# Kernel optimization log

Hardware: AMD Instinct MI355X
Metric: run time of the kernel (lower is better)

The kernel has to match this reference:

```python
import jax, jax.numpy as jnp
import numpy as np

B, C_IN, C_INTER, H, W_DIM = 8, 512, 256, 64, 64


def setup_inputs() -> dict:
    key = jax.random.key(0)
    k1, k2, k3, k4 = jax.random.split(key, 4)
    x = jax.random.normal(k1, (B, C_IN, H, W_DIM), dtype=jnp.float32)
    pem_feats = jax.random.normal(k2, (B, C_INTER, H * W_DIM), dtype=jnp.float32)
    # 1x1 conv weight stored as [out, in] (kernel spatial dims are 1x1)
    W = jax.random.normal(k3, (C_INTER, C_IN), dtype=jnp.float32) * (1.0 / np.sqrt(C_IN))
    bias = jax.random.normal(k4, (C_INTER,), dtype=jnp.float32) * 0.01
    return {"x": x, "pem_feats": pem_feats, "W": W, "bias": bias}


def reference(x, pem_feats, W, bias):
    b, c, h, w = x.shape
    # 1x1 conv == channel-mixing GEMM: [b, inter, h, w]
    proj = jnp.einsum('bchw,oc->bohw', x, W) + bias[None, :, None, None]
    proj = proj.reshape(b, -1, h * w)                      # [b, inter, hw]
    # weights[b,i,j] = <proj[:, i], pem[:, j]>  -> [b, hw, hw], softmax over j
    scores = jnp.einsum('bci,bcj->bij', proj, pem_feats)
    weights = jax.nn.softmax(scores, axis=-1)
    # out[b,k,i] = sum_j weights[b,j,i] * pem[b,k,j]
    eam = jnp.einsum('bji,bkj->bki', weights, pem_feats)   # [b, inter, hw]
    return eam.reshape(b, -1, h, w)
```

## Files before the change

### kernel.cpp

```cpp
#include <hip/hip_runtime.h>
#include <math.h>

#define BATCH 8
#define CIN 512
#define CO 256
#define HW 4096
#define KT 32
#define NSEG 4
#define SEGC 32

typedef unsigned short ushort_t;
typedef unsigned int uint_t;
typedef __bf16 v8bf __attribute__((ext_vector_type(8)));
typedef _Float16 v8h __attribute__((ext_vector_type(8)));
typedef _Float16 v4h __attribute__((ext_vector_type(4)));
typedef float v4f __attribute__((ext_vector_type(4)));
typedef ushort_t u16x8 __attribute__((ext_vector_type(8)));

__device__ __forceinline__ ushort_t f2bf(float f) {
  uint_t u = __float_as_uint(f);
  u += 0x7FFFu + ((u >> 16) & 1u);
  return (ushort_t)(u >> 16);
}
__device__ __forceinline__ float bf2f(ushort_t h) {
  return __uint_as_float(((uint_t)h) << 16);
}
__device__ __forceinline__ ushort_t f2h(float f) {
  return __builtin_bit_cast(ushort_t, (_Float16)f);
}
__device__ __forceinline__ v4f mfma16(v8bf a, v8bf b, v4f c) {
  return __builtin_amdgcn_mfma_f32_16x16x32_bf16(a, b, c, 0, 0, 0);
}
__device__ __forceinline__ v4f mfma16h(v8h a, v8h b, v4f c) {
  return __builtin_amdgcn_mfma_f32_16x16x32_f16(a, b, c, 0, 0, 0);
}
__device__ __forceinline__ v8h lds_frag_h512(const unsigned char* base, int row, int cb) {
  uint4 v = *(const uint4*)(base + row * 512 + (((cb) ^ (row & 7)) << 4));
  return __builtin_bit_cast(v8h, v);
}
__device__ __forceinline__ v8h lds_frag_h128(const unsigned char* base, int row, int cb) {
  uint4 v = *(const uint4*)(base + row * 128 + (((cb) ^ (row & 7)) << 4));
  return __builtin_bit_cast(v8h, v);
}
__device__ __forceinline__ v8bf lds_frag128(const unsigned char* base, int row, int cb) {
  uint4 v = *(const uint4*)(base + row * 128 + (((cb) ^ (row & 7)) << 4));
  return __builtin_bit_cast(v8bf, v);
}
__device__ __forceinline__ void gll16(const void* g, void* l) {
  __builtin_amdgcn_global_load_lds(
      (const __attribute__((address_space(1))) unsigned int*)g,
      (__attribute__((address_space(3))) unsigned int*)l, 16, 0, 0);
}

__global__ __launch_bounds__(256) void k_w_split(
    const float* __restrict__ W, ushort_t* __restrict__ w_hi,
    ushort_t* __restrict__ w_lo) {
  int idx = blockIdx.x * 256 + threadIdx.x;
  size_t off = (size_t)idx * 8;
  float4 v0 = *(const float4*)&W[off];
  float4 v1 = *(const float4*)&W[off + 4];
  float f[8] = {v0.x, v0.y, v0.z, v0.w, v1.x, v1.y, v1.z, v1.w};
  u16x8 h, l;
#pragma unroll
  for (int j = 0; j < 8; ++j) {
    ushort_t hh = f2bf(f[j]);
    h[j] = hh;
    l[j] = f2bf(f[j] - bf2f(hh));
  }
  *(u16x8*)&w_hi[off] = h;
  *(u16x8*)&w_lo[off] = l;
}

__global__ __launch_bounds__(256) void k_tr_x(
    const float* __restrict__ x,
    ushort_t* __restrict__ xt_hi, ushort_t* __restrict__ xt_lo) {
  __shared__ float T[64][65];
  const int i0 = blockIdx.x * 64;
  const int c0 = blockIdx.y * 64;
  const int b  = blockIdx.z;
  const int t  = threadIdx.x;
  const int cl = t >> 4;
  const int i4 = (t & 15) * 4;
#pragma unroll
  for (int r = 0; r < 4; ++r) {
    int c = c0 + r * 16 + cl;
    size_t off = ((size_t)b * CIN + c) * HW + i0 + i4;
    float4 v = *(const float4*)&x[off];
    T[r * 16 + cl][i4 + 0] = v.x;
    T[r * 16 + cl][i4 + 1] = v.y;
    T[r * 16 + cl][i4 + 2] = v.z;
    T[r * 16 + cl][i4 + 3] = v.w;
  }
  __syncthreads();
  {
    int il = t >> 2;
    int cs = (t & 3) * 16;
    u16x8 h0, h1, l0, l1;
#pragma unroll
    for (int j = 0; j < 8; ++j) {
      float f = T[cs + j][il];
      ushort_t h = f2bf(f);
      h0[j] = h;
      l0[j] = f2bf(f - bf2f(h));
    }
#pragma unroll
    for (int j = 0; j < 8; ++j) {
      float f = T[cs + 8 + j][il];
      ushort_t h = f2bf(f);
      h1[j] = h;
      l1[j] = f2bf(f - bf2f(h));
    }
    size_t ro = ((size_t)b * HW + i0 + il) * CIN + c0 + cs;
    *(u16x8*)&xt_hi[ro]     = h0;
    *(u16x8*)&xt_hi[ro + 8] = h1;
    *(u16x8*)&xt_lo[ro]     = l0;
    *(u16x8*)&xt_lo[ro + 8] = l1;
  }
}

__global__ __launch_bounds__(256, 2) void k_proj_mfma(
    const ushort_t* __restrict__ xt_hi, const ushort_t* __restrict__ xt_lo,
    const ushort_t* __restrict__ w_hi, const ushort_t* __restrict__ w_lo,
    const float* __restrict__ bias, ushort_t* __restrict__ proj_h) {
  __shared__ __align__(16) unsigned char L[4][128 * 128];
  const int bid = blockIdx.x;
  const int b = bid & 7;
  const int rest = bid >> 3;
  const int xt = rest & 31;
  const int oh = rest >> 5;
  const int x0 = xt * 128;
  const int t = threadIdx.x;
  const int lane = t & 63, wave = t >> 6;

  v4f acc[2][8];
#pragma unroll
  for (int xf = 0; xf < 2; ++xf)
#pragma unroll
    for (int of = 0; of < 8; ++of) acc[xf][of] = (v4f){0.f, 0.f, 0.f, 0.f};

  float bias_of[8];
#pragma unroll
  for (int of = 0; of < 8; ++of)
    bias_of[of] = bias[oh * 128 + of * 16 + (lane & 15)];

  for (int ch = 0; ch < 8; ++ch) {
    const int c0 = ch * 64;
#pragma unroll
    for (int i = 0; i < 4; ++i) {
      int G = i * 256 + t;
      int r = G >> 3, sl = G & 7;
      int cg = (sl ^ (r & 7)) << 3;
      size_t xsrc = ((size_t)b * HW + x0 + r) * CIN + c0 + cg;
      size_t wsrc = ((size_t)(oh * 128 + r)) * CIN + c0 + cg;
      unsigned lb = (unsigned)((i * 256 + wave * 64) << 4);
      gll16(&xt_hi[xsrc], &L[0][lb]);
      gll16(&xt_lo[xsrc], &L[1][lb]);
      gll16(&w_hi[wsrc],  &L[2][lb]);
      gll16(&w_lo[wsrc],  &L[3][lb]);
    }
    __syncthreads();
#pragma unroll
    for (int st = 0; st < 2; ++st) {
      int cb = st * 4 + (lane >> 4);
      v8bf ah0 = lds_frag128(L[0], wave * 32 + (lane & 15), cb);
      v8bf ah1 = lds_frag128(L[0], wave * 32 + 16 + (lane & 15), cb);
      v8bf al0 = lds_frag128(L[1], wave * 32 + (lane & 15), cb);
      v8bf al1 = lds_frag128(L[1], wave * 32 + 16 + (lane & 15), cb);
#pragma unroll
      for (int of = 0; of < 8; ++of) {
        v8bf bh = lds_frag128(L[2], of * 16 + (lane & 15), cb);
        v8bf bl = lds_frag128(L[3], of * 16 + (lane & 15), cb);
        acc[0][of] = mfma16(ah0, bh, acc[0][of]);
        acc[0][of] = mfma16(ah0, bl, acc[0][of]);
        acc[0][of] = mfma16(al0, bh, acc[0][of]);
        acc[1][of] = mfma16(ah1, bh, acc[1][of]);
        acc[1][of] = mfma16(ah1, bl, acc[1][of]);
        acc[1][of] = mfma16(al1, bh, acc[1][of]);
      }
    }
    __syncthreads();
  }

  ushort_t* Th = (ushort_t*)&L[0][0];
#pragma unroll
  for (int xf = 0; xf < 2; ++xf)
#pragma unroll
    for (int of = 0; of < 8; ++of)
#pragma unroll
      for (int r = 0; r < 4; ++r) {
        int x_loc = wave * 32 + xf * 16 + (lane >> 4) * 4 + r;
        int o_loc = of * 16 + (lane & 15);
        Th[x_loc * 128 + o_loc] = f2h(acc[xf][of][r] + bias_of[of]);
      }
  __syncthreads();
  {
    int row = t >> 1, half = t & 1;
    size_t off = ((size_t)b * HW + x0 + row) * CO + oh * 128 + half * 64;
#pragma unroll
    for (int j = 0; j < 8; ++j)
      *(uint4*)&proj_h[off + j * 8] =
          *(const uint4*)&Th[row * 128 + half * 64 + j * 8];
  }
}

__global__ __launch_bounds__(256) void k_tr_pem(
    const float* __restrict__ pem,
    ushort_t* __restrict__ pem_t_h, ushort_t* __restrict__ pem_h) {
  __shared__ float T[64][65];
  const int y0 = blockIdx.x * 64;
  const int c0 = blockIdx.y * 64;
  const int b  = blockIdx.z;
  const int t  = threadIdx.x;
  const int cl = t >> 4;
  const int y4 = (t & 15) * 4;
#pragma unroll
  for (int r = 0; r < 4; ++r) {
    int c = c0 + r * 16 + cl;
    size_t off = ((size_t)b * CO + c) * HW + y0 + y4;
    float4 v = *(const float4*)&pem[off];
    ushort4 h;
    h.x = f2h(v.x); h.y = f2h(v.y); h.z = f2h(v.z); h.w = f2h(v.w);
    *(ushort4*)&pem_h[off] = h;
    T[r * 16 + cl][y4 + 0] = v.x;
    T[r * 16 + cl][y4 + 1] = v.y;
    T[r * 16 + cl][y4 + 2] = v.z;
    T[r * 16 + cl][y4 + 3] = v.w;
  }
  __syncthreads();
  {
    int yl = t >> 2;
    int cs = (t & 3) * 16;
    u16x8 h0, h1;
#pragma unroll
    for (int j = 0; j < 8; ++j) h0[j] = f2h(T[cs + j][yl]);
#pragma unroll
    for (int j = 0; j < 8; ++j) h1[j] = f2h(T[cs + 8 + j][yl]);
    size_t ro = ((size_t)b * HW + y0 + yl) * CO + c0 + cs;
    *(u16x8*)&pem_t_h[ro]     = h0;
    *(u16x8*)&pem_t_h[ro + 8] = h1;
  }
}

__global__ __launch_bounds__(256, 2) void k_stats_f16(
    const ushort_t* __restrict__ proj_h, const ushort_t* __restrict__ pem_t_h,
    float* __restrict__ m_seg, float* __restrict__ d_seg) {
  __shared__ __align__(16) unsigned char pbuf[2][32 * 512];
  const int id = blockIdx.x;
  const int b = id & 7;
  const int rest = id >> 3;
  const int xt = rest & 15;
  const int seg = rest >> 4;
  const int x0 = xt * 256;
  const int t = threadIdx.x;
  const int lane = t & 63, wave = t >> 6;
  const int xw = x0 + wave * 64;

  v8h Ah[4][8];
#pragma unroll
  for (int xf = 0; xf < 4; ++xf) {
    const size_t ro =
        ((size_t)b * HW + xw + xf * 16 + (lane & 15)) * CO + (lane >> 4) * 8;
#pragma unroll
    for (int st = 0; st < 8; ++st)
      Ah[xf][st] = __builtin_bit_cast(v8h, *(const uint4*)&proj_h[ro + st * 32]);
  }

  float m[4][4], d[4][4];
#pragma unroll
  for (int xf = 0; xf < 4; ++xf)
#pragma unroll
    for (int r = 0; r < 4; ++r) { m[xf][r] = -3.0e38f; d[xf][r] = 0.f; }

  auto stage = [&](int bufi, int tt) {
    const int yy0 = tt * 32;
#pragma unroll
    for (int i = 0; i < 4; ++i) {
      int G = i * 256 + t;
      int r = G >> 5, sl = G & 31;
      size_t so = ((size_t)b * HW + yy0 + r) * CO + ((sl ^ (r & 7)) << 3);
      unsigned lb = (unsigned)((i * 256 + wave * 64) << 4);
      gll16(&pem_t_h[so], &pbuf[bufi][lb]);
    }
  };

  const int tt0 = seg * SEGC;
  stage(0, tt0);
  __syncthreads();

  for (int tc = 0; tc < SEGC; ++tc) {
    if (tc + 1 < SEGC) stage((tc + 1) & 1, tt0 + tc + 1);

    const unsigned char* bp = pbuf[tc & 1];
    v4f acc[4][2];
#pragma unroll
    for (int xf = 0; xf < 4; ++xf)
#pragma unroll
      for (int yc = 0; yc < 2; ++yc) acc[xf][yc] = (v4f){0.f, 0.f, 0.f, 0.f};

#pragma unroll
    for (int st = 0; st < 8; ++st) {
#pragma unroll
      for (int yc = 0; yc < 2; ++yc) {
        v8h bh = lds_frag_h512(bp, yc * 16 + (lane & 15), st * 4 + (lane >> 4));
        acc[0][yc] = mfma16h(Ah[0][st], bh, acc[0][yc]);
        acc[1][yc] = mfma16h(Ah[1][st], bh, acc[1][yc]);
        acc[2][yc] = mfma16h(Ah[2][st], bh, acc[2][yc]);
        acc[3][yc] = mfma16h(Ah[3][st], bh, acc[3][yc]);
      }
    }

#pragma unroll
    for (int xf = 0; xf < 4; ++xf) {
      float mx8 = fmaxf(fmaxf(fmaxf(acc[xf][0][0], acc[xf][0][1]),
                              fmaxf(acc[xf][0][2], acc[xf][0][3])),
                        fmaxf(fmaxf(acc[xf][1][0], acc[xf][1][1]),
                              fmaxf(acc[xf][1][2], acc[xf][1][3])));
      float minm = fminf(fminf(m[xf][0], m[xf][1]), fminf(m[xf][2], m[xf][3]));
      if (__any(mx8 > minm + 8.0f)) {
#pragma unroll
        for (int r = 0; r < 4; ++r) {
          float rm = fmaxf(acc[xf][0][r], acc[xf][1][r]);
          rm = fmaxf(rm, __shfl_xor(rm, 1));
          rm = fmaxf(rm, __shfl_xor(rm, 2));
          rm = fmaxf(rm, __shfl_xor(rm, 4));
          rm = fmaxf(rm, __shfl_xor(rm, 8));
          float mn = fmaxf(m[xf][r], rm);
          d[xf][r] *= __expf(m[xf][r] - mn);
          m[xf][r] = mn;
        }
      }
#pragma unroll
      for (int r = 0; r < 4; ++r)
        d[xf][r] += __expf(acc[xf][0][r] - m[xf][r]) +
                    __expf(acc[xf][1][r] - m[xf][r]);
    }
    __syncthreads();
  }

#pragma unroll
  for (int xf = 0; xf < 4; ++xf) {
    float dv[4];
#pragma unroll
    for (int r = 0; r < 4; ++r) {
      float v = d[xf][r];
      v += __shfl_xor(v, 1);
      v += __shfl_xor(v, 2);
      v += __shfl_xor(v, 4);
      v += __shfl_xor(v, 8);
      dv[r] = v;
    }
    if ((lane & 15) == 0) {
      size_t o = ((size_t)(b * NSEG + seg)) * HW + xw + xf * 16 + (lane >> 4) * 4;
      *(float4*)&m_seg[o] = make_float4(m[xf][0], m[xf][1], m[xf][2], m[xf][3]);
      *(float4*)&d_seg[o] = make_float4(dv[0], dv[1], dv[2], dv[3]);
    }
  }
}

__global__ __launch_bounds__(256) void k_red2(
    const float* __restrict__ m_seg, const float* __restrict__ d_seg,
    float* __restrict__ Cx) {
  int idx = blockIdx.x * 256 + threadIdx.x;
  int b = idx >> 12;
  int xx = idx & 4095;
  float ms[NSEG], ds[NSEG];
  float mm = -3.0e38f;
#pragma unroll
  for (int s = 0; s < NSEG; ++s) {
    ms[s] = m_seg[((size_t)(b * NSEG + s)) * HW + xx];
    ds[s] = d_seg[((size_t)(b * NSEG + s)) * HW + xx];
    mm = fmaxf(mm, ms[s]);
  }
  float dd = 0.f;
#pragma unroll
  for (int s = 0; s < NSEG; ++s) dd += ds[s] * __expf(ms[s] - mm);
  Cx[(size_t)b * HW + xx] = mm + __logf(dd);
}

__global__ __launch_bounds__(256, 2) void k_fused(
    const ushort_t* __restrict__ proj_h, const ushort_t* __restrict__ pem_t_h,
    const ushort_t* __restrict__ pem_h, const float* __restrict__ Cx,
    float* __restrict__ out) {
  __shared__ __align__(16) unsigned char Lp[64 * 512];
  __shared__ __align__(16) unsigned char Lk[256 * 128];
  __shared__ __align__(16) unsigned char Le[64 * 128];
  __shared__ float Clds[64];
  const int id = blockIdx.x;
  const int b = id & 7;
  const int yt = id >> 3;
  const int y0 = yt * 64;
  const int t = threadIdx.x;
  const int lane = t & 63, wave = t >> 6;

  v8h Bres[8];
  {
    const size_t ro =
        ((size_t)b * HW + y0 + wave * 16 + (lane & 15)) * CO + (lane >> 4) * 8;
#pragma unroll
    for (int st = 0; st < 8; ++st)
      Bres[st] = __builtin_bit_cast(v8h, *(const uint4*)&pem_t_h[ro + st * 32]);
  }

  v4f pv[4][4];
#pragma unroll
  for (int kf = 0; kf < 4; ++kf)
#pragma unroll
    for (int yf = 0; yf < 4; ++yf) pv[kf][yf] = (v4f){0.f, 0.f, 0.f, 0.f};

  for (int xt = 0; xt < 64; ++xt) {
    const int x0 = xt * 64;
    __syncthreads();
#pragma unroll
    for (int i = 0; i < 8; ++i) {
      int G = i * 256 + t;
      int r = G >> 5, sl = G & 31;
      size_t so = ((size_t)b * HW + x0 + r) * CO + ((sl ^ (r & 7)) << 3);
      gll16(&proj_h[so], &Lp[(unsigned)((i * 256 + wave * 64) << 4)]);
    }
#pragma unroll
    for (int i = 0; i < 8; ++i) {
      int G = i * 256 + t;
      int r = G >> 3, sl = G & 7;
      size_t so = ((size_t)b * CO + r) * HW + x0 + ((sl ^ (r & 7)) << 3);
      gll16(&pem_h[so], &Lk[(unsigned)((i * 256 + wave * 64) << 4)]);
    }
    if (t < 64) Clds[t] = Cx[(size_t)b * HW + x0 + t];
    __syncthreads();

    v4f s[4];
#pragma unroll
    for (int xf = 0; xf < 4; ++xf) s[xf] = (v4f){0.f, 0.f, 0.f, 0.f};
#pragma unroll
    for (int st = 0; st < 8; ++st) {
      int cb = st * 4 + (lane >> 4);
      v8h bh = Bres[st];
      s[0] = mfma16h(lds_frag_h512(Lp, 0  + (lane & 15), cb), bh, s[0]);
      s[1] = mfma16h(lds_frag_h512(Lp, 16 + (lane & 15), cb), bh, s[1]);
      s[2] = mfma16h(lds_frag_h512(Lp, 32 + (lane & 15), cb), bh, s[2]);
      s[3] = mfma16h(lds_frag_h512(Lp, 48 + (lane & 15), cb), bh, s[3]);
    }
    {
      int yl = wave * 16 + (lane & 15);
      int half = (lane >> 4) & 1;
      int gbase = (lane >> 4) >> 1;
#pragma unroll
      for (int xf = 0; xf < 4; ++xf) {
        float4 c4 = *(const float4*)&Clds[xf * 16 + (lane >> 4) * 4];
        float cc[4] = {c4.x, c4.y, c4.z, c4.w};
        v4h p;
#pragma unroll
        for (int r = 0; r < 4; ++r) p[r] = (_Float16)__expf(s[xf][r] - cc[r]);
        int gx = xf * 2 + gbase;
        *(uint2*)(Le + yl * 128 + ((gx ^ (yl & 7)) << 4) + half * 8) =
            __builtin_bit_cast(uint2, p);
      }
    }
    __syncthreads();

    const int kb = wave * 64;
#pragma unroll
    for (int ks = 0; ks < 2; ++ks) {
      int cb = ks * 4 + (lane >> 4);
      v8h e0 = lds_frag_h128(Le, 0  + (lane & 15), cb);
      v8h e1 = lds_frag_h128(Le, 16 + (lane & 15), cb);
      v8h e2 = lds_frag_h128(Le, 32 + (lane & 15), cb);
      v8h e3 = lds_frag_h128(Le, 48 + (lane & 15), cb);
#pragma unroll
      for (int kf = 0; kf < 4; ++kf) {
        v8h af = lds_frag_h128(Lk, kb + kf * 16 + (lane & 15), cb);
        pv[kf][0] = mfma16h(af, e0, pv[kf][0]);
        pv[kf][1] = mfma16h(af, e1, pv[kf][1]);
        pv[kf][2] = mfma16h(af, e2, pv[kf][2]);
        pv[kf][3] = mfma16h(af, e3, pv[kf][3]);
      }
    }
  }

#pragma unroll
  for (int kf = 0; kf < 4; ++kf)
#pragma unroll
    for (int yf = 0; yf < 4; ++yf)
#pragma unroll
      for (int r = 0; r < 4; ++r) {
        int k = wave * 64 + kf * 16 + (lane >> 4) * 4 + r;
        int y = y0 + yf * 16 + (lane & 15);
        out[((size_t)b * CO + k) * HW + y] = pv[kf][yf][r];
      }
}

__global__ __launch_bounds__(256) void k_proj(
    const float* __restrict__ x, const float* __restrict__ W,
    const float* __restrict__ bias, float* __restrict__ proj) {
  __shared__ float As[KT][68];
  __shared__ float Bs[KT][68];
  const int i0 = blockIdx.x * 64;
  const int o0 = blockIdx.y * 64;
  const int b  = blockIdx.z;
  const int t  = threadIdx.x;
  const int tx = t & 15, ty = t >> 4;
  const float* xb = x + (size_t)b * CIN * HW;
  float acc[4][4] = {};
  for (int c0 = 0; c0 < CIN; c0 += KT) {
#pragma unroll
    for (int l = 0; l < 8; ++l) {
      int idx = t + l * 256;
      int o = idx >> 5;
      int c = idx & 31;
      As[c][o] = W[(size_t)(o0 + o) * CIN + c0 + c];
    }
#pragma unroll
    for (int l = 0; l < 2; ++l) {
      int idx4 = t + l * 256;
      int c = idx4 >> 4;
      int i4 = idx4 & 15;
      *(float4*)&Bs[c][i4 * 4] =
          *(const float4*)&xb[(size_t)(c0 + c) * HW + i0 + i4 * 4];
    }
    __syncthreads();
#pragma unroll
    for (int c = 0; c < KT; ++c) {
      float4 a  = *(const float4*)&As[c][tx * 4];
      float4 bv = *(const float4*)&Bs[c][ty * 4];
      float av[4] = {a.x, a.y, a.z, a.w};
      float bb[4] = {bv.x, bv.y, bv.z, bv.w};
#pragma unroll
      for (int u = 0; u < 4; ++u)
#pragma unroll
        for (int v = 0; v < 4; ++v) acc[u][v] += av[u] * bb[v];
    }
    __syncthreads();
  }
  float* pbout = proj + (size_t)b * CO * HW;
#pragma unroll
  for (int u = 0; u < 4; ++u) {
    int o = o0 + tx * 4 + u;
    float bsv = bias[o];
    float4 r;
    r.x = acc[u][0] + bsv; r.y = acc[u][1] + bsv;
    r.z = acc[u][2] + bsv; r.w = acc[u][3] + bsv;
    *(float4*)&pbout[(size_t)o * HW + i0 + ty * 4] = r;
  }
}

__global__ __launch_bounds__(256) void k_stats(
    const float* __restrict__ proj, const float* __restrict__ pem,
    float* __restrict__ Mx, float* __restrict__ Dinv) {
  __shared__ float As[KT][68];
  __shared__ float Bs[KT][68];
  __shared__ float MsS[64][17];
  __shared__ float DsS[64][17];
  const int x0 = blockIdx.x * 64;
  const int b  = blockIdx.y;
  const int t  = threadIdx.x;
  const int tx = t & 15, ty = t >> 4;
  const float* pj = proj + (size_t)b * CO * HW;
  const float* pe = pem + (size_t)b * CO * HW;
  float m[4], d[4];
#pragma unroll
  for (int u = 0; u < 4; ++u) { m[u] = -3.0e38f; d[u] = 0.f; }
  for (int y0 = 0; y0 < HW; y0 += 64) {
    float s[4][4] = {};
    for (int c0 = 0; c0 < CO; c0 += KT) {
#pragma unroll
      for (int l = 0; l < 2; ++l) {
        int idx4 = t + l * 256;
        int c = idx4 >> 4, w4 = idx4 & 15;
        *(float4*)&As[c][w4 * 4] =
            *(const float4*)&pj[(size_t)(c0 + c) * HW + x0 + w4 * 4];
        *(float4*)&Bs[c][w4 * 4] =
            *(const float4*)&pe[(size_t)(c0 + c) * HW + y0 + w4 * 4];
      }
      __syncthreads();
#pragma unroll
      for (int c = 0; c < KT; ++c) {
        float4 a  = *(const float4*)&As[c][tx * 4];
        float4 bv = *(const float4*)&Bs[c][ty * 4];
        float av[4] = {a.x, a.y, a.z, a.w};
        float bb[4] = {bv.x, bv.y, bv.z, bv.w};
#pragma unroll
        for (int u = 0; u < 4; ++u)
#pragma unroll
          for (int v = 0; v < 4; ++v) s[u][v] += av[u] * bb[v];
      }
      __syncthreads();
    }
#pragma unroll
    for (int u = 0; u < 4; ++u) {
      float mv = fmaxf(fmaxf(s[u][0], s[u][1]), fmaxf(s[u][2], s[u][3]));
      if (mv > m[u]) { d[u] *= __expf(m[u] - mv); m[u] = mv; }
      d[u] += __expf(s[u][0] - m[u]) + __expf(s[u][1] - m[u]) +
              __expf(s[u][2] - m[u]) + __expf(s[u][3] - m[u]);
    }
  }
#pragma unroll
  for (int u = 0; u < 4; ++u) { MsS[tx * 4 + u][ty] = m[u]; DsS[tx * 4 + u][ty] = d[u]; }
  __syncthreads();
  if (t < 64) {
    float mm = -3.0e38f;
#pragma unroll
    for (int i = 0; i < 16; ++i) mm = fmaxf(mm, MsS[t][i]);
    float dd = 0.f;
#pragma unroll
    for (int i = 0; i < 16; ++i) dd += DsS[t][i] * __expf(MsS[t][i] - mm);
    Mx[(size_t)b * HW + x0 + t]   = mm;
    Dinv[(size_t)b * HW + x0 + t] = 1.0f / dd;
  }
}

__global__ __launch_bounds__(256) void k_out(
    const float* __restrict__ proj, const float* __restrict__ pem,
    const float* __restrict__ Mx, const float* __restrict__ Dinv,
    float* __restrict__ out) {
  __shared__ float As[KT][68];
  __shared__ float Bs[KT][68];
  __shared__ float E[64][68];
  const int y0 = blockIdx.x * 64;
  const int b  = blockIdx.y;
  const int t  = threadIdx.x;
  const int tx = t & 15, ty = t >> 4;
  const int kg = t >> 3, yg = t & 7;
  const float* pj = proj + (size_t)b * CO * HW;
  const float* pe = pem + (size_t)b * CO * HW;
  const float* Mb = Mx + (size_t)b * HW;
  const float* Db = Dinv + (size_t)b * HW;
  float acc[8][8] = {};
  for (int x0 = 0; x0 < HW; x0 += 64) {
    float s[4][4] = {};
    for (int c0 = 0; c0 < CO; c0 += KT) {
#pragma unroll
      for (int l = 0; l < 2; ++l) {
        int idx4 = t + l * 256;
        int c = idx4 >> 4, w4 = idx4 & 15;
        *(float4*)&As[c][w4 * 4] =
            *(const float4*)&pj[(size_t)(c0 + c) * HW + x0 + w4 * 4];
        *(float4*)&Bs[c][w4 * 4] =
            *(const float4*)&pe[(size_t)(c0 + c) * HW + y0 + w4 * 4];
      }
      __syncthreads();
#pragma unroll
      for (int c = 0; c < KT; ++c) {
        float4 a  = *(const float4*)&As[c][tx * 4];
        float4 bv = *(const float4*)&Bs[c][ty * 4];
        float av[4] = {a.x, a.y, a.z, a.w};
        float bb[4] = {bv.x, bv.y, bv.z, bv.w};
#pragma unroll
        for (int u = 0; u < 4; ++u)
#pragma unroll
          for (int v = 0; v < 4; ++v) s[u][v] += av[u] * bb[v];
      }
      __syncthreads();
    }
#pragma unroll
    for (int u = 0; u < 4; ++u) {
      int xr = x0 + tx * 4 + u;
      float mm = Mb[xr];
      float di = Db[xr];
      E[tx * 4 + u][ty * 4 + 0] = __expf(s[u][0] - mm) * di;
      E[tx * 4 + u][ty * 4 + 1] = __expf(s[u][1] - mm) * di;
      E[tx * 4 + u][ty * 4 + 2] = __expf(s[u][2] - mm) * di;
      E[tx * 4 + u][ty * 4 + 3] = __expf(s[u][3] - mm) * di;
    }
    __syncthreads();
    for (int xi = 0; xi < 64; xi += 4) {
      float4 p[8];
#pragma unroll
      for (int u = 0; u < 8; ++u)
        p[u] = *(const float4*)&pe[(size_t)(kg * 8 + u) * HW + x0 + xi];
#pragma unroll
      for (int j = 0; j < 4; ++j) {
        float4 e0 = *(const float4*)&E[xi + j][yg * 8];
        float4 e1 = *(const float4*)&E[xi + j][yg * 8 + 4];
        float evv[8] = {e0.x, e0.y, e0.z, e0.w, e1.x, e1.y, e1.z, e1.w};
#pragma unroll
        for (int u = 0; u < 8; ++u) {
          float a = (j == 0) ? p[u].x : (j == 1) ? p[u].y : (j == 2) ? p[u].z : p[u].w;
#pragma unroll
          for (int v = 0; v < 8; ++v) acc[u][v] += a * evv[v];
        }
      }
    }
    __syncthreads();
  }
#pragma unroll
  for (int u = 0; u < 8; ++u) {
    int k = kg * 8 + u;
    float4 r0, r1;
    r0.x = acc[u][0]; r0.y = acc[u][1]; r0.z = acc[u][2]; r0.w = acc[u][3];
    r1.x = acc[u][4]; r1.y = acc[u][5]; r1.z = acc[u][6]; r1.w = acc[u][7];
    float* ob = out + ((size_t)b * CO + k) * HW + y0 + yg * 8;
    *(float4*)&ob[0] = r0;
    *(float4*)&ob[4] = r1;
  }
}

extern "C" void kernel_launch(void* const* d_in, const int* in_sizes, int n_in,
                              void* d_out, int out_size, void* d_ws, size_t ws_size,
                              hipStream_t stream) {
  const float* x    = (const float*)d_in[0];
  const float* pem  = (const float*)d_in[1];
  const float* W    = (const float*)d_in[2];
  const float* bias = (const float*)d_in[3];
  float* out = (float*)d_out;

  const size_t NS   = (size_t)BATCH * HW * CO;
  const size_t NS2  = (size_t)BATCH * HW * CIN;
  const size_t HWB  = (size_t)BATCH * HW;
  const size_t SEGN = (size_t)BATCH * NSEG * HW;
  const size_t WN   = (size_t)CO * CIN;

  unsigned char* basep = (unsigned char*)d_ws;
  ushort_t* proj_h   = (ushort_t*)basep;
  ushort_t* pem_t_h  = proj_h + NS;
  ushort_t* pem_h    = pem_t_h + NS;
  float*    Cxp      = (float*)(pem_h + NS);
  float*    m_seg    = Cxp + HWB;
  float*    d_seg    = m_seg + SEGN;
  ushort_t* xt_hi    = (ushort_t*)(d_seg + SEGN);
  ushort_t* xt_lo    = xt_hi + NS2;
  ushort_t* w_hi     = xt_lo + NS2;
  ushort_t* w_lo     = w_hi + WN;

  const size_t need = 3 * NS * 2 + HWB * 4 + 2 * SEGN * 4 + 2 * NS2 * 2 + 2 * WN * 2;

  if (ws_size < need) {
    float* proj = (float*)d_ws;
    float* Mx2  = proj + NS;
    float* Di2  = Mx2 + HWB;
    const size_t need_f = (NS + 2 * HWB) * sizeof(float);
    if (ws_size < need_f) return;
    k_proj <<<dim3(HW / 64, CO / 64, BATCH), 256, 0, stream>>>(x, W, bias, proj);
    k_stats<<<dim3(HW / 64, BATCH),          256, 0, stream>>>(proj, pem, Mx2, Di2);
    k_out  <<<dim3(HW / 64, BATCH),          256, 0, stream>>>(proj, pem, Mx2, Di2, out);
    return;
  }

  k_w_split<<<64, 256, 0, stream>>>(W, w_hi, w_lo);
  k_tr_x<<<dim3(HW / 64, CIN / 64, BATCH), 256, 0, stream>>>(x, xt_hi, xt_lo);
  k_proj_mfma<<<512, 256, 0, stream>>>(xt_hi, xt_lo, w_hi, w_lo, bias, proj_h);
  k_tr_pem<<<dim3(HW / 64, CO / 64, BATCH), 256, 0, stream>>>(pem, pem_t_h, pem_h);

  k_stats_f16<<<512, 256, 0, stream>>>(proj_h, pem_t_h, m_seg, d_seg);
  k_red2<<<128, 256, 0, stream>>>(m_seg, d_seg, Cxp);
  k_fused<<<512, 256, 0, stream>>>(proj_h, pem_t_h, pem_h, Cxp, out);
}
```

Measured before the change: 369.8 us.

## Use single fp16 projection GEMM, widen attention blocks to 512 threads with double buffering

The split bf16 hi/lo projection (three MFMAs per tile) becomes a single fp16 MFMA path, which removes the lo buffers and two thirds of the projection math and traffic. k_stats_f16 and k_fused now run 512-thread blocks covering larger tiles. k_fused double-buffers the proj/pem LDS stages so the next tile loads during the PV MFMAs, and it reads Cx straight from global instead of staging it in LDS. Projection accuracy drops to fp16, and the larger LDS footprint may reduce occupancy.

```diff
diff --git a/kernel.cpp b/kernel.cpp
--- a/kernel.cpp
+++ b/kernel.cpp
@@ -11,25 +11,13 @@
 
 typedef unsigned short ushort_t;
 typedef unsigned int uint_t;
-typedef __bf16 v8bf __attribute__((ext_vector_type(8)));
 typedef _Float16 v8h __attribute__((ext_vector_type(8)));
 typedef _Float16 v4h __attribute__((ext_vector_type(4)));
 typedef float v4f __attribute__((ext_vector_type(4)));
 typedef ushort_t u16x8 __attribute__((ext_vector_type(8)));
 
-__device__ __forceinline__ ushort_t f2bf(float f) {
-  uint_t u = __float_as_uint(f);
-  u += 0x7FFFu + ((u >> 16) & 1u);
-  return (ushort_t)(u >> 16);
-}
-__device__ __forceinline__ float bf2f(ushort_t h) {
-  return __uint_as_float(((uint_t)h) << 16);
-}
 __device__ __forceinline__ ushort_t f2h(float f) {
   return __builtin_bit_cast(ushort_t, (_Float16)f);
-}
-__device__ __forceinline__ v4f mfma16(v8bf a, v8bf b, v4f c) {
-  return __builtin_amdgcn_mfma_f32_16x16x32_bf16(a, b, c, 0, 0, 0);
 }
 __device__ __forceinline__ v4f mfma16h(v8h a, v8h b, v4f c) {
   return __builtin_amdgcn_mfma_f32_16x16x32_f16(a, b, c, 0, 0, 0);
@@ -41,10 +29,6 @@
 __device__ __forceinline__ v8h lds_frag_h128(const unsigned char* base, int row, int cb) {
   uint4 v = *(const uint4*)(base + row * 128 + (((cb) ^ (row & 7)) << 4));
   return __builtin_bit_cast(v8h, v);
-}
-__device__ __forceinline__ v8bf lds_frag128(const unsigned char* base, int row, int cb) {
-  uint4 v = *(const uint4*)(base + row * 128 + (((cb) ^ (row & 7)) << 4));
-  return __builtin_bit_cast(v8bf, v);
 }
 __device__ __forceinline__ void gll16(const void* g, void* l) {
   __builtin_amdgcn_global_load_lds(
@@ -52,28 +36,21 @@
       (__attribute__((address_space(3))) unsigned int*)l, 16, 0, 0);
 }
 
-__global__ __launch_bounds__(256) void k_w_split(
-    const float* __restrict__ W, ushort_t* __restrict__ w_hi,
-    ushort_t* __restrict__ w_lo) {
+__global__ __launch_bounds__(256) void k_w(
+    const float* __restrict__ W, ushort_t* __restrict__ w_h) {
   int idx = blockIdx.x * 256 + threadIdx.x;
   size_t off = (size_t)idx * 8;
   float4 v0 = *(const float4*)&W[off];
   float4 v1 = *(const float4*)&W[off + 4];
   float f[8] = {v0.x, v0.y, v0.z, v0.w, v1.x, v1.y, v1.z, v1.w};
-  u16x8 h, l;
-#pragma unroll
-  for (int j = 0; j < 8; ++j) {
-    ushort_t hh = f2bf(f[j]);
-    h[j] = hh;
-    l[j] = f2bf(f[j] - bf2f(hh));
-  }
-  *(u16x8*)&w_hi[off] = h;
-  *(u16x8*)&w_lo[off] = l;
+  u16x8 h;
+#pragma unroll
+  for (int j = 0; j < 8; ++j) h[j] = f2h(f[j]);
+  *(u16x8*)&w_h[off] = h;
 }
 
 __global__ __launch_bounds__(256) void k_tr_x(
-    const float* __restrict__ x,
-    ushort_t* __restrict__ xt_hi, ushort_t* __restrict__ xt_lo) {
+    const float* __restrict__ x, ushort_t* __restrict__ xt_h) {
   __shared__ float T[64][65];
   const int i0 = blockIdx.x * 64;
   const int c0 = blockIdx.y * 64;
@@ -95,34 +72,21 @@
   {
     int il = t >> 2;
     int cs = (t & 3) * 16;
-    u16x8 h0, h1, l0, l1;
-#pragma unroll
-    for (int j = 0; j < 8; ++j) {
-      float f = T[cs + j][il];
-      ushort_t h = f2bf(f);
-      h0[j] = h;
-      l0[j] = f2bf(f - bf2f(h));
-    }
-#pragma unroll
-    for (int j = 0; j < 8; ++j) {
-      float f = T[cs + 8 + j][il];
-      ushort_t h = f2bf(f);
-      h1[j] = h;
-      l1[j] = f2bf(f - bf2f(h));
-    }
+    u16x8 h0, h1;
+#pragma unroll
+    for (int j = 0; j < 8; ++j) h0[j] = f2h(T[cs + j][il]);
+#pragma unroll
+    for (int j = 0; j < 8; ++j) h1[j] = f2h(T[cs + 8 + j][il]);
     size_t ro = ((size_t)b * HW + i0 + il) * CIN + c0 + cs;
-    *(u16x8*)&xt_hi[ro]     = h0;
-    *(u16x8*)&xt_hi[ro + 8] = h1;
-    *(u16x8*)&xt_lo[ro]     = l0;
-    *(u16x8*)&xt_lo[ro + 8] = l1;
+    *(u16x8*)&xt_h[ro]     = h0;
+    *(u16x8*)&xt_h[ro + 8] = h1;
   }
 }
 
 __global__ __launch_bounds__(256, 2) void k_proj_mfma(
-    const ushort_t* __restrict__ xt_hi, const ushort_t* __restrict__ xt_lo,
-    const ushort_t* __restrict__ w_hi, const ushort_t* __restrict__ w_lo,
+    const ushort_t* __restrict__ xt_h, const ushort_t* __restrict__ w_h,
     const float* __restrict__ bias, ushort_t* __restrict__ proj_h) {
-  __shared__ __align__(16) unsigned char L[4][128 * 128];
+  __shared__ __align__(16) unsigned char L[2][128 * 128];
   const int bid = blockIdx.x;
   const int b = bid & 7;
   const int rest = bid >> 3;
@@ -153,29 +117,20 @@
       size_t xsrc = ((size_t)b * HW + x0 + r) * CIN + c0 + cg;
       size_t wsrc = ((size_t)(oh * 128 + r)) * CIN + c0 + cg;
       unsigned lb = (unsigned)((i * 256 + wave * 64) << 4);
-      gll16(&xt_hi[xsrc], &L[0][lb]);
-      gll16(&xt_lo[xsrc], &L[1][lb]);
-      gll16(&w_hi[wsrc],  &L[2][lb]);
-      gll16(&w_lo[wsrc],  &L[3][lb]);
+      gll16(&xt_h[xsrc], &L[0][lb]);
+      gll16(&w_h[wsrc],  &L[1][lb]);
     }
     __syncthreads();
 #pragma unroll
     for (int st = 0; st < 2; ++st) {
       int cb = st * 4 + (lane >> 4);
-      v8bf ah0 = lds_frag128(L[0], wave * 32 + (lane & 15), cb);
-      v8bf ah1 = lds_frag128(L[0], wave * 32 + 16 + (lane & 15), cb);
-      v8bf al0 = lds_frag128(L[1], wave * 32 + (lane & 15), cb);
-      v8bf al1 = lds_frag128(L[1], wave * 32 + 16 + (lane & 15), cb);
+      v8h ah0 = lds_frag_h128(L[0], wave * 32 + (lane & 15), cb);
+      v8h ah1 = lds_frag_h128(L[0], wave * 32 + 16 + (lane & 15), cb);
 #pragma unroll
       for (int of = 0; of < 8; ++of) {
-        v8bf bh = lds_frag128(L[2], of * 16 + (lane & 15), cb);
-        v8bf bl = lds_frag128(L[3], of * 16 + (lane & 15), cb);
-        acc[0][of] = mfma16(ah0, bh, acc[0][of]);
-        acc[0][of] = mfma16(ah0, bl, acc[0][of]);
-        acc[0][of] = mfma16(al0, bh, acc[0][of]);
-        acc[1][of] = mfma16(ah1, bh, acc[1][of]);
-        acc[1][of] = mfma16(ah1, bl, acc[1][of]);
-        acc[1][of] = mfma16(al1, bh, acc[1][of]);
+        v8h bh = lds_frag_h128(L[1], of * 16 + (lane & 15), cb);
+        acc[0][of] = mfma16h(ah0, bh, acc[0][of]);
+        acc[1][of] = mfma16h(ah1, bh, acc[1][of]);
       }
     }
     __syncthreads();
@@ -241,16 +196,16 @@
   }
 }
 
-__global__ __launch_bounds__(256, 2) void k_stats_f16(
+__global__ __launch_bounds__(512, 2) void k_stats_f16(
     const ushort_t* __restrict__ proj_h, const ushort_t* __restrict__ pem_t_h,
     float* __restrict__ m_seg, float* __restrict__ d_seg) {
   __shared__ __align__(16) unsigned char pbuf[2][32 * 512];
   const int id = blockIdx.x;
   const int b = id & 7;
   const int rest = id >> 3;
-  const int xt = rest & 15;
-  const int seg = rest >> 4;
-  const int x0 = xt * 256;
+  const int xt = rest & 7;
+  const int seg = rest >> 3;
+  const int x0 = xt * 512;
   const int t = threadIdx.x;
   const int lane = t & 63, wave = t >> 6;
   const int xw = x0 + wave * 64;
@@ -274,11 +229,11 @@
   auto stage = [&](int bufi, int tt) {
     const int yy0 = tt * 32;
 #pragma unroll
-    for (int i = 0; i < 4; ++i) {
-      int G = i * 256 + t;
+    for (int i = 0; i < 2; ++i) {
+      int G = i * 512 + t;
       int r = G >> 5, sl = G & 31;
       size_t so = ((size_t)b * HW + yy0 + r) * CO + ((sl ^ (r & 7)) << 3);
-      unsigned lb = (unsigned)((i * 256 + wave * 64) << 4);
+      unsigned lb = (unsigned)((i * 512 + wave * 64) << 4);
       gll16(&pem_t_h[so], &pbuf[bufi][lb]);
     }
   };
@@ -377,18 +332,17 @@
   Cx[(size_t)b * HW + xx] = mm + __logf(dd);
 }
 
-__global__ __launch_bounds__(256, 2) void k_fused(
+__global__ __launch_bounds__(512, 2) void k_fused(
     const ushort_t* __restrict__ proj_h, const ushort_t* __restrict__ pem_t_h,
     const ushort_t* __restrict__ pem_h, const float* __restrict__ Cx,
     float* __restrict__ out) {
-  __shared__ __align__(16) unsigned char Lp[64 * 512];
-  __shared__ __align__(16) unsigned char Lk[256 * 128];
-  __shared__ __align__(16) unsigned char Le[64 * 128];
-  __shared__ float Clds[64];
+  __shared__ __align__(16) unsigned char Lp[2][64 * 512];
+  __shared__ __align__(16) unsigned char Lk[2][256 * 128];
+  __shared__ __align__(16) unsigned char Le[128 * 128];
   const int id = blockIdx.x;
   const int b = id & 7;
   const int yt = id >> 3;
-  const int y0 = yt * 64;
+  const int y0 = yt * 128;
   const int t = threadIdx.x;
   const int lane = t & 63, wave = t >> 6;
 
@@ -401,30 +355,35 @@
       Bres[st] = __builtin_bit_cast(v8h, *(const uint4*)&pem_t_h[ro + st * 32]);
   }
 
-  v4f pv[4][4];
-#pragma unroll
-  for (int kf = 0; kf < 4; ++kf)
-#pragma unroll
-    for (int yf = 0; yf < 4; ++yf) pv[kf][yf] = (v4f){0.f, 0.f, 0.f, 0.f};
-
-  for (int xt = 0; xt < 64; ++xt) {
+  v4f pv[2][8];
+#pragma unroll
+  for (int kf = 0; kf < 2; ++kf)
+#pragma unroll
+    for (int yf = 0; yf < 8; ++yf) pv[kf][yf] = (v4f){0.f, 0.f, 0.f, 0.f};
+
+  auto stage = [&](int bufi, int xt) {
     const int x0 = xt * 64;
-    __syncthreads();
-#pragma unroll
-    for (int i = 0; i < 8; ++i) {
-      int G = i * 256 + t;
+#pragma unroll
+    for (int i = 0; i < 4; ++i) {
+      int G = i * 512 + t;
       int r = G >> 5, sl = G & 31;
       size_t so = ((size_t)b * HW + x0 + r) * CO + ((sl ^ (r & 7)) << 3);
-      gll16(&proj_h[so], &Lp[(unsigned)((i * 256 + wave * 64) << 4)]);
-    }
-#pragma unroll
-    for (int i = 0; i < 8; ++i) {
-      int G = i * 256 + t;
+      gll16(&proj_h[so], &Lp[bufi][(unsigned)((i * 512 + wave * 64) << 4)]);
+    }
+#pragma unroll
+    for (int i = 0; i < 4; ++i) {
+      int G = i * 512 + t;
       int r = G >> 3, sl = G & 7;
       size_t so = ((size_t)b * CO + r) * HW + x0 + ((sl ^ (r & 7)) << 3);
-      gll16(&pem_h[so], &Lk[(unsigned)((i * 256 + wave * 64) << 4)]);
-    }
-    if (t < 64) Clds[t] = Cx[(size_t)b * HW + x0 + t];
+      gll16(&pem_h[so], &Lk[bufi][(unsigned)((i * 512 + wave * 64) << 4)]);
+    }
+  };
+
+  stage(0, 0);
+
+  for (int xt = 0; xt < 64; ++xt) {
+    const int cur = xt & 1;
+    const int x0 = xt * 64;
     __syncthreads();
 
     v4f s[4];
@@ -434,10 +393,10 @@
     for (int st = 0; st < 8; ++st) {
       int cb = st * 4 + (lane >> 4);
       v8h bh = Bres[st];
-      s[0] = mfma16h(lds_frag_h512(Lp, 0  + (lane & 15), cb), bh, s[0]);
-      s[1] = mfma16h(lds_frag_h512(Lp, 16 + (lane & 15), cb), bh, s[1]);
-      s[2] = mfma16h(lds_frag_h512(Lp, 32 + (lane & 15), cb), bh, s[2]);
-      s[3] = mfma16h(lds_frag_h512(Lp, 48 + (lane & 15), cb), bh, s[3]);
+      s[0] = mfma16h(lds_frag_h512(Lp[cur], 0  + (lane & 15), cb), bh, s[0]);
+      s[1] = mfma16h(lds_frag_h512(Lp[cur], 16 + (lane & 15), cb), bh, s[1]);
+      s[2] = mfma16h(lds_frag_h512(Lp[cur], 32 + (lane & 15), cb), bh, s[2]);
+      s[3] = mfma16h(lds_frag_h512(Lp[cur], 48 + (lane & 15), cb), bh, s[3]);
     }
     {
       int yl = wave * 16 + (lane & 15);
@@ -445,7 +404,8 @@
       int gbase = (lane >> 4) >> 1;
 #pragma unroll
       for (int xf = 0; xf < 4; ++xf) {
-        float4 c4 = *(const float4*)&Clds[xf * 16 + (lane >> 4) * 4];
+        float4 c4 = *(const float4*)&Cx[(size_t)b * HW + x0 + xf * 16 +
+                                        (lane >> 4) * 4];
         float cc[4] = {c4.x, c4.y, c4.z, c4.w};
         v4h p;
 #pragma unroll
@@ -457,32 +417,33 @@
     }
     __syncthreads();
 
-    const int kb = wave * 64;
+    if (xt + 1 < 64) stage(cur ^ 1, xt + 1);
+
+    const int kb = wave * 32;
 #pragma unroll
     for (int ks = 0; ks < 2; ++ks) {
       int cb = ks * 4 + (lane >> 4);
-      v8h e0 = lds_frag_h128(Le, 0  + (lane & 15), cb);
-      v8h e1 = lds_frag_h128(Le, 16 + (lane & 15), cb);
-      v8h e2 = lds_frag_h128(Le, 32 + (lane & 15), cb);
-      v8h e3 = lds_frag_h128(Le, 48 + (lane & 15), cb);
-#pragma unroll
-      for (int kf = 0; kf < 4; ++kf) {
-        v8h af = lds_frag_h128(Lk, kb + kf * 16 + (lane & 15), cb);
-        pv[kf][0] = mfma16h(af, e0, pv[kf][0]);
-        pv[kf][1] = mfma16h(af, e1, pv[kf][1]);
-        pv[kf][2] = mfma16h(af, e2, pv[kf][2]);
-        pv[kf][3] = mfma16h(af, e3, pv[kf][3]);
-      }
-    }
-  }
-
-#pragma unroll
-  for (int kf = 0; kf < 4; ++kf)
-#pragma unroll
-    for (int yf = 0; yf < 4; ++yf)
+      v8h e[8];
+#pragma unroll
+      for (int yf = 0; yf < 8; ++yf)
+        e[yf] = lds_frag_h128(Le, yf * 16 + (lane & 15), cb);
+#pragma unroll
+      for (int kf = 0; kf < 2; ++kf) {
+        v8h af = lds_frag_h128(Lk[cur], kb + kf * 16 + (lane & 15), cb);
+#pragma unroll
+        for (int yf = 0; yf < 8; ++yf)
+          pv[kf][yf] = mfma16h(af, e[yf], pv[kf][yf]);
+      }
+    }
+  }
+
+#pragma unroll
+  for (int kf = 0; kf < 2; ++kf)
+#pragma unroll
+    for (int yf = 0; yf < 8; ++yf)
 #pragma unroll
       for (int r = 0; r < 4; ++r) {
-        int k = wave * 64 + kf * 16 + (lane >> 4) * 4 + r;
+        int k = wave * 32 + kf * 16 + (lane >> 4) * 4 + r;
         int y = y0 + yf * 16 + (lane & 15);
         out[((size_t)b * CO + k) * HW + y] = pv[kf][yf][r];
       }
@@ -715,12 +676,10 @@
   float*    Cxp      = (float*)(pem_h + NS);
   float*    m_seg    = Cxp + HWB;
   float*    d_seg    = m_seg + SEGN;
-  ushort_t* xt_hi    = (ushort_t*)(d_seg + SEGN);
-  ushort_t* xt_lo    = xt_hi + NS2;
-  ushort_t* w_hi     = xt_lo + NS2;
-  ushort_t* w_lo     = w_hi + WN;
-
-  const size_t need = 3 * NS * 2 + HWB * 4 + 2 * SEGN * 4 + 2 * NS2 * 2 + 2 * WN * 2;
+  ushort_t* xt_h     = (ushort_t*)(d_seg + SEGN);
+  ushort_t* w_h      = xt_h + NS2;
+
+  const size_t need = 3 * NS * 2 + HWB * 4 + 2 * SEGN * 4 + NS2 * 2 + WN * 2;
 
   if (ws_size < need) {
     float* proj = (float*)d_ws;
@@ -734,12 +693,12 @@
     return;
   }
 
-  k_w_split<<<64, 256, 0, stream>>>(W, w_hi, w_lo);
-  k_tr_x<<<dim3(HW / 64, CIN / 64, BATCH), 256, 0, stream>>>(x, xt_hi, xt_lo);
-  k_proj_mfma<<<512, 256, 0, stream>>>(xt_hi, xt_lo, w_hi, w_lo, bias, proj_h);
+  k_w<<<64, 256, 0, stream>>>(W, w_h);
+  k_tr_x<<<dim3(HW / 64, CIN / 64, BATCH), 256, 0, stream>>>(x, xt_h);
+  k_proj_mfma<<<512, 256, 0, stream>>>(xt_h, w_h, bias, proj_h);
   k_tr_pem<<<dim3(HW / 64, CO / 64, BATCH), 256, 0, stream>>>(pem, pem_t_h, pem_h);
 
-  k_stats_f16<<<512, 256, 0, stream>>>(proj_h, pem_t_h, m_seg, d_seg);
+  k_stats_f16<<<256, 512, 0, stream>>>(proj_h, pem_t_h, m_seg, d_seg);
   k_red2<<<128, 256, 0, stream>>>(m_seg, d_seg, Cxp);
-  k_fused<<<512, 256, 0, stream>>>(proj_h, pem_t_h, pem_h, Cxp, out);
-}
+  k_fused<<<256, 512, 0, stream>>>(proj_h, pem_t_h, pem_h, Cxp, out);
+}
```

Result: faster. 327.2 us (-11.5%).
